# Performance work log

Hardware: AMD Instinct MI355X
Metric: run time of the kernel (lower is better)

The kernel has to match this reference:

```python
import jax, jax.numpy as jnp
import numpy as np

N_USER = 100000
N_ITEM = 100000
N_TAG = 10000
DIM = 128
E_BUYS = 1_000_000
E_REV = 1_000_000
E_TAGS = 1_000_000
W_SCALE = 0.05


def setup_inputs() -> dict:
    key = jax.random.key(0)
    ks = jax.random.split(key, 18)
    inp = {
        "x_user": jax.random.normal(ks[0], (N_USER, DIM), jnp.float32),
        "x_item": jax.random.normal(ks[1], (N_ITEM, DIM), jnp.float32),
        "x_tag": jax.random.normal(ks[2], (N_TAG, DIM), jnp.float32),
        # edge_index per relation: row 0 = src node ids, row 1 = dst node ids
        "ei_buys": jnp.stack([
            jax.random.randint(ks[3], (E_BUYS,), 0, N_USER, jnp.int32),
            jax.random.randint(ks[4], (E_BUYS,), 0, N_ITEM, jnp.int32)]),
        "ei_rev": jnp.stack([
            jax.random.randint(ks[5], (E_REV,), 0, N_ITEM, jnp.int32),
            jax.random.randint(ks[6], (E_REV,), 0, N_USER, jnp.int32)]),
        "ei_tags": jnp.stack([
            jax.random.randint(ks[7], (E_TAGS,), 0, N_TAG, jnp.int32),
            jax.random.randint(ks[8], (E_TAGS,), 0, N_ITEM, jnp.int32)]),
    }
    # SAGEConv params per edge type: lin_l (neighbor agg), lin_r (root), bias
    names = ["buys", "rev", "tags"]
    for i, n in enumerate(names):
        inp[f"Wl_{n}"] = jax.random.normal(ks[9 + 3 * i], (DIM, DIM), jnp.float32) * W_SCALE
        inp[f"Wr_{n}"] = jax.random.normal(ks[10 + 3 * i], (DIM, DIM), jnp.float32) * W_SCALE
        inp[f"b_{n}"] = jnp.zeros((DIM,), jnp.float32)
    return inp


def _sage(x_src, x_dst, ei, Wl, Wr, b):
    """SAGEConv with mean neighbor aggregation: lin_l(mean_j x_j) + lin_r(x_i) + b."""
    n_dst = x_dst.shape[0]
    src, dst = ei[0], ei[1]
    msg_sum = jax.ops.segment_sum(x_src[src], dst, num_segments=n_dst)  # [n_dst, D]
    cnt = jax.ops.segment_sum(jnp.ones(src.shape, x_src.dtype), dst, num_segments=n_dst)
    msg_mean = msg_sum / jnp.maximum(cnt, 1.0)[:, None]
    return msg_mean @ Wl + x_dst @ Wr + b


def reference(x_user, x_item, x_tag, ei_buys, ei_rev, ei_tags,
              Wl_buys, Wr_buys, b_buys,
              Wl_rev, Wr_rev, b_rev,
              Wl_tags, Wr_tags, b_tags):
    # per-relation SAGEConv
    o_item_buys = _sage(x_user, x_item, ei_buys, Wl_buys, Wr_buys, b_buys)
    o_user = _sage(x_item, x_user, ei_rev, Wl_rev, Wr_rev, b_rev)
    o_item_tags = _sage(x_tag, x_item, ei_tags, Wl_tags, Wr_tags, b_tags)
    # HeteroConv aggr='mean' across edge types per destination node type
    out_item = 0.5 * (o_item_buys + o_item_tags)
    out_user = o_user  # single relation into 'user'
    return (out_user, out_item)
```

## Files before the change

kernel.cpp:

```cpp
#include <hip/hip_runtime.h>
#include <hip/hip_bf16.h>
#include <stdint.h>

#define DIM 128
#define NNODE 100000
#define NB 196
#define NBT (3 * NB)
#define T_TILE 4096

typedef __attribute__((ext_vector_type(8))) short short8;
typedef __attribute__((ext_vector_type(4))) float f32x4;

__device__ __forceinline__ unsigned short f32_to_bf16_rne(float f) {
    union { float f; uint32_t u; } v; v.f = f;
    uint32_t u = v.u;
    uint32_t r = u + 0x7FFFu + ((u >> 16) & 1u);
    return (unsigned short)(r >> 16);
}
__device__ __forceinline__ float bf16_to_f32(unsigned short u) {
    union { uint32_t i; float f; } v; v.i = ((uint32_t)u) << 16; return v.f;
}

__global__ __launch_bounds__(256) void coarse_hist(
    const int* __restrict__ ei0, const int* __restrict__ ei1, const int* __restrict__ ei2,
    int E0, int E1, int E2, int* __restrict__ ccnt) {
    __shared__ int h[NBT];
    int Etot = E0 + E1 + E2;
    for (int i = threadIdx.x; i < NBT; i += 256) h[i] = 0;
    __syncthreads();
    for (int e = blockIdx.x * blockDim.x + threadIdx.x; e < Etot; e += gridDim.x * blockDim.x) {
        int rel, le; const int* ei; int E;
        if (e < E0)           { rel = 0; le = e;           ei = ei0; E = E0; }
        else if (e < E0 + E1) { rel = 1; le = e - E0;      ei = ei1; E = E1; }
        else                  { rel = 2; le = e - E0 - E1; ei = ei2; E = E2; }
        int d = ei[E + le];
        atomicAdd(&h[rel * NB + (d >> 9)], 1);
    }
    __syncthreads();
    for (int i = threadIdx.x; i < NBT; i += 256) {
        int c = h[i];
        if (c) atomicAdd(&ccnt[i], c);
    }
}

__global__ __launch_bounds__(1024) void coarse_scan(const int* __restrict__ ccnt,
                                                    int* __restrict__ bases,
                                                    int* __restrict__ cursor) {
    __shared__ int s[1024];
    int t = threadIdx.x;
    int v = (t < NBT) ? ccnt[t] : 0;
    s[t] = v;
    __syncthreads();
    for (int d = 1; d < 1024; d <<= 1) {
        int x = (t >= d) ? s[t - d] : 0;
        __syncthreads();
        s[t] += x;
        __syncthreads();
    }
    int excl = s[t] - v;
    if (t < NBT) { bases[t] = excl; cursor[t] = excl; }
    if (t == NBT) bases[NBT] = excl;
}

__global__ __launch_bounds__(256) void coarse_scatter(
    const int* __restrict__ ei0, const int* __restrict__ ei1, const int* __restrict__ ei2,
    int E0, int E1, int E2, int* __restrict__ cursor, int* __restrict__ pairs) {
    __shared__ int h[NBT], hb[NBT], lc[NBT];
    int Etot = E0 + E1 + E2;
    int ntiles = (Etot + T_TILE - 1) / T_TILE;
    for (int tile = blockIdx.x; tile < ntiles; tile += gridDim.x) {
        int tbase = tile * T_TILE;
        for (int i = threadIdx.x; i < NBT; i += 256) { h[i] = 0; lc[i] = 0; }
        __syncthreads();
        int binreg[16], valreg[16];
        #pragma unroll
        for (int k = 0; k < 16; k++) {
            int e = tbase + k * 256 + threadIdx.x;
            binreg[k] = -1;
            if (e < Etot) {
                int rel, le; const int* ei; int E;
                if (e < E0)           { rel = 0; le = e;           ei = ei0; E = E0; }
                else if (e < E0 + E1) { rel = 1; le = e - E0;      ei = ei1; E = E1; }
                else                  { rel = 2; le = e - E0 - E1; ei = ei2; E = E2; }
                int d = ei[E + le];
                int s = ei[le];
                int bin = rel * NB + (d >> 9);
                binreg[k] = bin;
                valreg[k] = s | ((d & 511) << 17);
                atomicAdd(&h[bin], 1);
            }
        }
        __syncthreads();
        for (int i = threadIdx.x; i < NBT; i += 256) {
            int c = h[i];
            hb[i] = c ? atomicAdd(&cursor[i], c) : 0;
        }
        __syncthreads();
        #pragma unroll
        for (int k = 0; k < 16; k++) {
            if (binreg[k] >= 0) {
                int bin = binreg[k];
                int pos = hb[bin] + atomicAdd(&lc[bin], 1);
                pairs[pos] = valreg[k];
            }
        }
        __syncthreads();
    }
}

__global__ __launch_bounds__(256) void fine_sort(
    const int* __restrict__ bases, const int* __restrict__ pairs,
    int* __restrict__ off, int* __restrict__ sorted, int N) {
    __shared__ int h[512], ho[512], ssum[256];
    int b = blockIdx.x;
    int rel = b / NB, jb = b - rel * NB;
    int ebase = bases[b], ne = bases[b + 1] - ebase;
    int dbase = jb << 9;
    int tid = threadIdx.x;
    for (int i = tid; i < 512; i += 256) h[i] = 0;
    __syncthreads();
    for (int i = tid; i < ne; i += 256) {
        int dl = pairs[ebase + i] >> 17;
        atomicAdd(&h[dl], 1);
    }
    __syncthreads();
    int v0 = h[tid * 2], v1 = h[tid * 2 + 1];
    int tsum = v0 + v1;
    ssum[tid] = tsum;
    __syncthreads();
    for (int s = 1; s < 256; s <<= 1) {
        int t = (tid >= s) ? ssum[tid - s] : 0;
        __syncthreads();
        ssum[tid] += t;
        __syncthreads();
    }
    int excl = ssum[tid] - tsum;
    ho[tid * 2] = excl;
    ho[tid * 2 + 1] = excl + v0;
    __syncthreads();
    for (int i = tid; i < 512; i += 256) {
        int d = dbase + i;
        if (d < N) off[rel * N + d] = ebase + ho[i];
        h[i] = 0;
    }
    __syncthreads();
    for (int i = tid; i < ne; i += 256) {
        int p = pairs[ebase + i];
        int dl = p >> 17;
        int pos = ebase + ho[dl] + atomicAdd(&h[dl], 1);
        sorted[pos] = p & 0x1FFFF;
    }
}

__global__ void pack_kernel(const float* __restrict__ Wl_b, const float* __restrict__ Wr_b,
                            const float* __restrict__ b_b,
                            const float* __restrict__ Wl_r, const float* __restrict__ Wr_r,
                            const float* __restrict__ b_r,
                            const float* __restrict__ Wl_t, const float* __restrict__ Wr_t,
                            const float* __restrict__ b_t,
                            unsigned short* __restrict__ pw_item,
                            unsigned short* __restrict__ pw_user,
                            float* __restrict__ bias_item, float* __restrict__ bias_user) {
    const int NI = 12 * 8 * 64 * 8;
    const int NU = 8 * 8 * 64 * 8;
    int o = blockIdx.x * blockDim.x + threadIdx.x;
    if (o < NI) {
        int j = o & 7, lane = (o >> 3) & 63, ks = o >> 12;
        int n = ((o >> 9) & 7) * 16 + (lane & 15);
        int k = (ks & 3) * 32 + (lane >> 4) * 8 + j;
        int src = ks >> 2;
        float v;
        if (src == 0)      v = 0.5f * Wl_b[k * DIM + n];
        else if (src == 1) v = 0.5f * Wl_t[k * DIM + n];
        else               v = 0.5f * (Wr_b[k * DIM + n] + Wr_t[k * DIM + n]);
        pw_item[o] = f32_to_bf16_rne(v);
    } else if (o < NI + NU) {
        int oo = o - NI;
        int j = oo & 7, lane = (oo >> 3) & 63, ks = oo >> 12;
        int n = ((oo >> 9) & 7) * 16 + (lane & 15);
        int k = (ks & 3) * 32 + (lane >> 4) * 8 + j;
        float v = ((ks >> 2) == 0) ? Wl_r[k * DIM + n] : Wr_r[k * DIM + n];
        pw_user[oo] = f32_to_bf16_rne(v);
    } else {
        int oo = o - NI - NU;
        if (oo < DIM)            bias_item[oo] = 0.5f * (b_b[oo] + b_t[oo]);
        else if (oo < 2 * DIM)   bias_user[oo - DIM] = b_r[oo - DIM];
    }
}

__device__ __forceinline__ void cg_product(
    unsigned char* stage, const short8* af,
    const unsigned short* __restrict__ pw, int slot0,
    const float* __restrict__ bias,
    unsigned short* __restrict__ dst, int g0, int lane) {
    const int quad = lane >> 4, l15 = lane & 15;
    f32x4 acc[8];
    #pragma unroll
    for (int i = 0; i < 8; i++) acc[i] = (f32x4){0.f, 0.f, 0.f, 0.f};
    #pragma unroll
    for (int ksl = 0; ksl < 4; ksl++) {
        const unsigned short* wp = pw + ((size_t)(slot0 + ksl) * 8 * 64 + lane) * 8;
        #pragma unroll
        for (int nt = 0; nt < 8; nt++) {
            short8 wfrag = *(const short8*)(wp + (size_t)nt * 64 * 8);
            acc[nt] = __builtin_amdgcn_mfma_f32_16x16x32_bf16(af[ksl], wfrag, acc[nt], 0, 0, 0);
        }
    }
    unsigned short* outb = (unsigned short*)stage;
    #pragma unroll
    for (int nt = 0; nt < 8; nt++) {
        float bv = bias ? bias[nt * 16 + l15] : 0.f;
        #pragma unroll
        for (int r = 0; r < 4; r++) {
            outb[(((quad << 2) + r) << 7) + (nt << 4) + l15] =
                f32_to_bf16_rne(acc[nt][r] + bv);
        }
    }
    unsigned char* mp = (unsigned char*)(dst + ((size_t)g0 << 7));
    #pragma unroll
    for (int s = 0; s < 4; s++) {
        uint4 vv = *(const uint4*)(stage + (s << 10) + (lane << 4));
        *(uint4*)(mp + (s << 10) + (lane << 4)) = vv;
    }
}

__global__ __launch_bounds__(256) void conv_gemm(
    const float* __restrict__ xu, const float* __restrict__ xi, const float* __restrict__ xt,
    const unsigned short* __restrict__ pw_item, const unsigned short* __restrict__ pw_user,
    const float* __restrict__ bias_item, const float* __restrict__ bias_user,
    unsigned short* __restrict__ yu, unsigned short* __restrict__ yi,
    unsigned short* __restrict__ yt,
    unsigned short* __restrict__ ru, unsigned short* __restrict__ ri,
    int GU, int GI, int GT) {
    __shared__ __align__(1024) unsigned char smem[4][4096];
    const int wid = threadIdx.x >> 6;
    const int lane = threadIdx.x & 63;
    const int grp = blockIdx.x * 4 + wid;
    if (grp >= GU + GI + GT) return;
    const float* src; const unsigned short *pwA, *pwB; const float* biasB;
    unsigned short *outA, *outB; int slotA, slotB, g0; bool two;
    if (grp < GU) {
        g0 = grp << 4; src = xu + ((size_t)g0 << 7);
        pwA = pw_item; slotA = 0; outA = yu;
        pwB = pw_user; slotB = 4; outB = ru; biasB = bias_user; two = true;
    } else if (grp < GU + GI) {
        g0 = (grp - GU) << 4; src = xi + ((size_t)g0 << 7);
        pwA = pw_user; slotA = 0; outA = yi;
        pwB = pw_item; slotB = 8; outB = ri; biasB = bias_item; two = true;
    } else {
        g0 = (grp - GU - GI) << 4; src = xt + ((size_t)g0 << 7);
        pwA = pw_item; slotA = 4; outA = yt; two = false;
        pwB = nullptr; outB = nullptr; biasB = nullptr; slotB = 0;
    }
    unsigned char* stage = smem[wid];
    #pragma unroll
    for (int s = 0; s < 8; s++) {
        float4 f = *(const float4*)((const unsigned char*)src + (s << 10) + (lane << 4));
        int row = (s << 1) + (lane >> 5);
        unsigned int b = ((unsigned int)row << 8) + ((unsigned int)(lane & 31) << 3);
        b ^= (unsigned int)((row & 15) << 4);
        ushort4 u;
        u.x = f32_to_bf16_rne(f.x); u.y = f32_to_bf16_rne(f.y);
        u.z = f32_to_bf16_rne(f.z); u.w = f32_to_bf16_rne(f.w);
        *(ushort4*)(stage + b) = u;
    }
    short8 af[4];
    const int quad = lane >> 4, l15 = lane & 15;
    #pragma unroll
    for (int ksl = 0; ksl < 4; ksl++) {
        unsigned int rb = ((unsigned int)l15 << 8) + (ksl << 6) + (quad << 4);
        rb ^= (unsigned int)(l15 << 4);
        af[ksl] = *(const short8*)(stage + rb);
    }
    cg_product(stage, af, pwA, slotA, nullptr, outA, g0, lane);
    if (two) cg_product(stage, af, pwB, slotB, biasB, outB, g0, lane);
}

__device__ __forceinline__ void gather_seg(
    const unsigned short* __restrict__ xs, const int* __restrict__ sorted,
    const int* bnd, unsigned char* stage, unsigned char* segb,
    int lane, int Etot, f32x4* acc) {
    const int b0 = bnd[0];
    const int L  = bnd[16] - b0;
    if (L <= 0) return;
    int nchunk = (L + 31) >> 5;
    if (nchunk > 20) nchunk = 20;
    const int tot = nchunk << 5;
    for (int i = lane; i < tot; i += 64) {
        int k = b0 + i;
        int s = 0;
        #pragma unroll
        for (int t = 1; t <= 16; t++) s += (k >= bnd[t]) ? 1 : 0;
        segb[i] = (unsigned char)s;
    }
    const int l15 = lane & 15;
    int deg = bnd[l15 + 1] - bnd[l15];
    const short ivb = (short)f32_to_bf16_rne(1.0f / (float)max(deg, 1));
    const int jsel = (lane & 7) >> 1;
    const int laneoff = ((lane >> 3) << 5) + ((lane & 1) << 4);
    const unsigned int stage_u =
        (unsigned int)(size_t)(__attribute__((address_space(3))) unsigned char*)stage;
    const unsigned int tbA = stage_u + ((lane >> 4) << 11) + ((lane & 15) << 3);
    const unsigned char* xsb = (const unsigned char*)xs;
    const int kmax = min(b0 + L - 1, Etot - 1);
    for (int c = 0; c < nchunk; c++) {
        int kk = min(b0 + (c << 5) + (lane & 31), kmax);
        const int sv = sorted[kk];
        #pragma unroll
        for (int q = 0; q < 8; q++) {
            int srow = __shfl(sv, (q << 2) + jsel, 64);
            const unsigned char* gp = xsb + (((size_t)srow) << 8) + laneoff;
            __builtin_amdgcn_global_load_lds(
                (const __attribute__((address_space(1))) unsigned int*)gp,
                (__attribute__((address_space(3))) unsigned int*)(stage + (q << 10)),
                16, 0, 0);
        }
        const unsigned long long sg =
            *(const unsigned long long*)(segb + (c << 5) + ((lane >> 4) << 3));
        short8 af;
        #pragma unroll
        for (int j = 0; j < 8; j++)
            af[j] = ((int)((sg >> (j << 3)) & 0xFFull) == l15) ? ivb : (short)0;
        asm volatile("s_waitcnt vmcnt(0)" ::: "memory");
        unsigned long long blo[8], bhi[8];
        #pragma unroll
        for (int nt = 0; nt < 8; nt++) {
            asm volatile("ds_read_b64_tr_b16 %0, %2\n\t"
                         "ds_read_b64_tr_b16 %1, %2 offset:1024"
                         : "=&v"(blo[nt]), "=&v"(bhi[nt]) : "v"(tbA + (nt << 7)));
        }
        asm volatile("s_waitcnt lgkmcnt(0)" ::: "memory");
        __builtin_amdgcn_sched_barrier(0);
        #pragma unroll
        for (int nt = 0; nt < 8; nt++) {
            union { unsigned long long u[2]; short8 s; } cv;
            cv.u[0] = blo[nt]; cv.u[1] = bhi[nt];
            acc[nt] = __builtin_amdgcn_mfma_f32_16x16x32_bf16(af, cv.s, acc[nt], 0, 0, 0);
        }
    }
}

__global__ __launch_bounds__(256) void agg_final(
    const unsigned short* __restrict__ yu, const unsigned short* __restrict__ yi,
    const unsigned short* __restrict__ yt,
    const unsigned short* __restrict__ ru, const unsigned short* __restrict__ ri,
    const int* __restrict__ sorted, const int* __restrict__ off,
    float* __restrict__ out, int N, int Etot) {
    __shared__ __align__(1024) unsigned char smem[4][9216];
    const int wid = threadIdx.x >> 6;
    const int lane = threadIdx.x & 63;
    const int grp = blockIdx.x * 4 + wid;
    const int Gi = N >> 4;
    if (grp >= 2 * Gi) return;
    unsigned char* stage = smem[wid];
    unsigned char* segb  = smem[wid] + 8192;
    int* bnd = (int*)(smem[wid] + 8192 + 640);
    const int quad = lane >> 4, l15 = lane & 15;

    f32x4 acc[8];
    #pragma unroll
    for (int i = 0; i < 8; i++) acc[i] = (f32x4){0.f, 0.f, 0.f, 0.f};

    float* op; const unsigned short* rt; int g0;
    if (grp < Gi) {
        g0 = grp << 4;
        if (lane < 17) bnd[lane] = off[g0 + lane];
        gather_seg(yu, sorted, bnd, stage, segb, lane, Etot, acc);
        if (lane < 17) { int idx = 2 * N + g0 + lane; bnd[lane] = (idx < 3 * N) ? off[idx] : Etot; }
        gather_seg(yt, sorted, bnd, stage, segb, lane, Etot, acc);
        op = out + (size_t)N * DIM; rt = ri;
    } else {
        g0 = (grp - Gi) << 4;
        if (lane < 17) bnd[lane] = off[N + g0 + lane];
        gather_seg(yi, sorted, bnd, stage, segb, lane, Etot, acc);
        op = out; rt = ru;
    }
    #pragma unroll
    for (int nt = 0; nt < 8; nt++) {
        #pragma unroll
        for (int r = 0; r < 4; r++) {
            size_t idx = (size_t)(g0 + (quad << 2) + r) * DIM + (nt << 4) + l15;
            op[idx] = acc[nt][r] + bf16_to_f32(rt[idx]);
        }
    }
}

extern "C" void kernel_launch(void* const* d_in, const int* in_sizes, int n_in,
                              void* d_out, int out_size, void* d_ws, size_t ws_size,
                              hipStream_t stream) {
    const float* x_user = (const float*)d_in[0];
    const float* x_item = (const float*)d_in[1];
    const float* x_tag  = (const float*)d_in[2];
    const int* ei_buys  = (const int*)d_in[3];
    const int* ei_rev   = (const int*)d_in[4];
    const int* ei_tags  = (const int*)d_in[5];
    const float* Wl_b = (const float*)d_in[6];
    const float* Wr_b = (const float*)d_in[7];
    const float* b_b  = (const float*)d_in[8];
    const float* Wl_r = (const float*)d_in[9];
    const float* Wr_r = (const float*)d_in[10];
    const float* b_r  = (const float*)d_in[11];
    const float* Wl_t = (const float*)d_in[12];
    const float* Wr_t = (const float*)d_in[13];
    const float* b_t  = (const float*)d_in[14];

    const int N  = NNODE;
    const int E0 = in_sizes[3] / 2, E1 = in_sizes[4] / 2, E2 = in_sizes[5] / 2;
    const int n_user = in_sizes[0] / DIM, n_item = in_sizes[1] / DIM, n_tag = in_sizes[2] / DIM;

    char* w = (char*)d_ws;
    int* off    = (int*)(w + 0);
    int* ccnt   = (int*)(w + 1200128);
    int* bases  = (int*)(w + 1202560);
    int* cursor = (int*)(w + 1204992);
    int* sorted = (int*)(w + 1207424);
    int* pairs  = (int*)(w + 13207424);
    unsigned short* pw_item = (unsigned short*)(w + 25207424);
    unsigned short* pw_user = (unsigned short*)(w + 25305728);
    float* bias_item = (float*)(w + 25371264);
    float* bias_user = (float*)(w + 25371776);
    unsigned short* yu = (unsigned short*)(w + 25372288);
    unsigned short* yi = (unsigned short*)(w + 50972288);
    unsigned short* yt = (unsigned short*)(w + 76572288);
    unsigned short* ru = (unsigned short*)(w + 79132288);
    unsigned short* ri = (unsigned short*)(w + 104732288);

    float* out_all = (float*)d_out;

    int Etot = E0 + E1 + E2;

    hipMemsetAsync(ccnt, 0, NBT * sizeof(int), stream);

    pack_kernel<<<(49152 + 32768 + 2 * DIM + 255) / 256, 256, 0, stream>>>(
        Wl_b, Wr_b, b_b, Wl_r, Wr_r, b_r, Wl_t, Wr_t, b_t,
        pw_item, pw_user, bias_item, bias_user);

    int GU = n_user / 16, GI = n_item / 16, GT = n_tag / 16;
    conv_gemm<<<(GU + GI + GT + 3) / 4, 256, 0, stream>>>(
        x_user, x_item, x_tag, pw_item, pw_user, bias_item, bias_user,
        yu, yi, yt, ru, ri, GU, GI, GT);

    coarse_hist<<<512, 256, 0, stream>>>(ei_buys, ei_rev, ei_tags, E0, E1, E2, ccnt);

    coarse_scan<<<1, 1024, 0, stream>>>(ccnt, bases, cursor);

    int ntiles = (Etot + T_TILE - 1) / T_TILE;
    coarse_scatter<<<ntiles, 256, 0, stream>>>(
        ei_buys, ei_rev, ei_tags, E0, E1, E2, cursor, pairs);

    fine_sort<<<NBT, 256, 0, stream>>>(bases, pairs, off, sorted, N);

    int ngrp = 2 * (N / 16);
    agg_final<<<(ngrp + 3) / 4, 256, 0, stream>>>(
        yu, yi, yt, ru, ri, sorted, off, out_all, N, Etot);
}
```

Measured before the change: 423.1 us.

## Fuse coarse histogram into conv GEMM launch and fold counter reset into pack

The coarse destination histogram is merged into the conv GEMM kernel as 512 extra leading blocks, so the two independent stages share one launch and can overlap on the GPU. The memset of the bucket counters moves into pack_kernel, removing a separate memset launch. The GEMM A-fragment load now reads fp32 rows straight from global memory into registers and converts them to bf16, skipping the LDS staging round-trip. The direct per-lane row loads are less coalesced than the old staged 1 KB strided loads, which could raise memory transaction cost for the 210k-row input read.

```diff
diff --git a/kernel.cpp b/kernel.cpp
--- a/kernel.cpp
+++ b/kernel.cpp
@@ -7,6 +7,7 @@
 #define NB 196
 #define NBT (3 * NB)
 #define T_TILE 4096
+#define NHIST 512
 
 typedef __attribute__((ext_vector_type(8))) short short8;
 typedef __attribute__((ext_vector_type(4))) float f32x4;
@@ -19,28 +20,6 @@
 }
 __device__ __forceinline__ float bf16_to_f32(unsigned short u) {
     union { uint32_t i; float f; } v; v.i = ((uint32_t)u) << 16; return v.f;
-}
-
-__global__ __launch_bounds__(256) void coarse_hist(
-    const int* __restrict__ ei0, const int* __restrict__ ei1, const int* __restrict__ ei2,
-    int E0, int E1, int E2, int* __restrict__ ccnt) {
-    __shared__ int h[NBT];
-    int Etot = E0 + E1 + E2;
-    for (int i = threadIdx.x; i < NBT; i += 256) h[i] = 0;
-    __syncthreads();
-    for (int e = blockIdx.x * blockDim.x + threadIdx.x; e < Etot; e += gridDim.x * blockDim.x) {
-        int rel, le; const int* ei; int E;
-        if (e < E0)           { rel = 0; le = e;           ei = ei0; E = E0; }
-        else if (e < E0 + E1) { rel = 1; le = e - E0;      ei = ei1; E = E1; }
-        else                  { rel = 2; le = e - E0 - E1; ei = ei2; E = E2; }
-        int d = ei[E + le];
-        atomicAdd(&h[rel * NB + (d >> 9)], 1);
-    }
-    __syncthreads();
-    for (int i = threadIdx.x; i < NBT; i += 256) {
-        int c = h[i];
-        if (c) atomicAdd(&ccnt[i], c);
-    }
 }
 
 __global__ __launch_bounds__(1024) void coarse_scan(const int* __restrict__ ccnt,
@@ -160,10 +139,12 @@
                             const float* __restrict__ b_t,
                             unsigned short* __restrict__ pw_item,
                             unsigned short* __restrict__ pw_user,
-                            float* __restrict__ bias_item, float* __restrict__ bias_user) {
+                            float* __restrict__ bias_item, float* __restrict__ bias_user,
+                            int* __restrict__ ccnt) {
     const int NI = 12 * 8 * 64 * 8;
     const int NU = 8 * 8 * 64 * 8;
     int o = blockIdx.x * blockDim.x + threadIdx.x;
+    if (o < NBT) ccnt[o] = 0;
     if (o < NI) {
         int j = o & 7, lane = (o >> 3) & 63, ks = o >> 12;
         int n = ((o >> 9) & 7) * 16 + (lane & 15);
@@ -224,18 +205,40 @@
     }
 }
 
-__global__ __launch_bounds__(256) void conv_gemm(
+__global__ __launch_bounds__(256) void prep_kernel(
     const float* __restrict__ xu, const float* __restrict__ xi, const float* __restrict__ xt,
     const unsigned short* __restrict__ pw_item, const unsigned short* __restrict__ pw_user,
     const float* __restrict__ bias_item, const float* __restrict__ bias_user,
     unsigned short* __restrict__ yu, unsigned short* __restrict__ yi,
     unsigned short* __restrict__ yt,
     unsigned short* __restrict__ ru, unsigned short* __restrict__ ri,
-    int GU, int GI, int GT) {
-    __shared__ __align__(1024) unsigned char smem[4][4096];
+    int GU, int GI, int GT,
+    const int* __restrict__ ei0, const int* __restrict__ ei1, const int* __restrict__ ei2,
+    int E0, int E1, int E2, int* __restrict__ ccnt) {
+    __shared__ __align__(1024) unsigned char smem[16384];
+    if (blockIdx.x < NHIST) {
+        int* h = (int*)smem;
+        int Etot = E0 + E1 + E2;
+        for (int i = threadIdx.x; i < NBT; i += 256) h[i] = 0;
+        __syncthreads();
+        for (int e = blockIdx.x * 256 + threadIdx.x; e < Etot; e += NHIST * 256) {
+            int rel, le; const int* ei; int E;
+            if (e < E0)           { rel = 0; le = e;           ei = ei0; E = E0; }
+            else if (e < E0 + E1) { rel = 1; le = e - E0;      ei = ei1; E = E1; }
+            else                  { rel = 2; le = e - E0 - E1; ei = ei2; E = E2; }
+            int d = ei[E + le];
+            atomicAdd(&h[rel * NB + (d >> 9)], 1);
+        }
+        __syncthreads();
+        for (int i = threadIdx.x; i < NBT; i += 256) {
+            int c = h[i];
+            if (c) atomicAdd(&ccnt[i], c);
+        }
+        return;
+    }
     const int wid = threadIdx.x >> 6;
     const int lane = threadIdx.x & 63;
-    const int grp = blockIdx.x * 4 + wid;
+    const int grp = (blockIdx.x - NHIST) * 4 + wid;
     if (grp >= GU + GI + GT) return;
     const float* src; const unsigned short *pwA, *pwB; const float* biasB;
     unsigned short *outA, *outB; int slotA, slotB, g0; bool two;
@@ -252,25 +255,21 @@
         pwA = pw_item; slotA = 4; outA = yt; two = false;
         pwB = nullptr; outB = nullptr; biasB = nullptr; slotB = 0;
     }
-    unsigned char* stage = smem[wid];
-    #pragma unroll
-    for (int s = 0; s < 8; s++) {
-        float4 f = *(const float4*)((const unsigned char*)src + (s << 10) + (lane << 4));
-        int row = (s << 1) + (lane >> 5);
-        unsigned int b = ((unsigned int)row << 8) + ((unsigned int)(lane & 31) << 3);
-        b ^= (unsigned int)((row & 15) << 4);
-        ushort4 u;
-        u.x = f32_to_bf16_rne(f.x); u.y = f32_to_bf16_rne(f.y);
-        u.z = f32_to_bf16_rne(f.z); u.w = f32_to_bf16_rne(f.w);
-        *(ushort4*)(stage + b) = u;
-    }
+    unsigned char* stage = smem + wid * 4096;
+    const int quad = lane >> 4, l15 = lane & 15;
+    const float* rowp = src + (size_t)l15 * DIM;
     short8 af[4];
-    const int quad = lane >> 4, l15 = lane & 15;
     #pragma unroll
     for (int ksl = 0; ksl < 4; ksl++) {
-        unsigned int rb = ((unsigned int)l15 << 8) + (ksl << 6) + (quad << 4);
-        rb ^= (unsigned int)(l15 << 4);
-        af[ksl] = *(const short8*)(stage + rb);
+        const float* p = rowp + ksl * 32 + quad * 8;
+        float4 a = *(const float4*)p;
+        float4 b = *(const float4*)(p + 4);
+        short8 f;
+        f[0] = (short)f32_to_bf16_rne(a.x); f[1] = (short)f32_to_bf16_rne(a.y);
+        f[2] = (short)f32_to_bf16_rne(a.z); f[3] = (short)f32_to_bf16_rne(a.w);
+        f[4] = (short)f32_to_bf16_rne(b.x); f[5] = (short)f32_to_bf16_rne(b.y);
+        f[6] = (short)f32_to_bf16_rne(b.z); f[7] = (short)f32_to_bf16_rne(b.w);
+        af[ksl] = f;
     }
     cg_product(stage, af, pwA, slotA, nullptr, outA, g0, lane);
     if (two) cg_product(stage, af, pwB, slotB, biasB, outB, g0, lane);
@@ -429,18 +428,16 @@
 
     int Etot = E0 + E1 + E2;
 
-    hipMemsetAsync(ccnt, 0, NBT * sizeof(int), stream);
-
     pack_kernel<<<(49152 + 32768 + 2 * DIM + 255) / 256, 256, 0, stream>>>(
         Wl_b, Wr_b, b_b, Wl_r, Wr_r, b_r, Wl_t, Wr_t, b_t,
-        pw_item, pw_user, bias_item, bias_user);
+        pw_item, pw_user, bias_item, bias_user, ccnt);
 
     int GU = n_user / 16, GI = n_item / 16, GT = n_tag / 16;
-    conv_gemm<<<(GU + GI + GT + 3) / 4, 256, 0, stream>>>(
+    int conv_blocks = (GU + GI + GT + 3) / 4;
+    prep_kernel<<<NHIST + conv_blocks, 256, 0, stream>>>(
         x_user, x_item, x_tag, pw_item, pw_user, bias_item, bias_user,
-        yu, yi, yt, ru, ri, GU, GI, GT);
-
-    coarse_hist<<<512, 256, 0, stream>>>(ei_buys, ei_rev, ei_tags, E0, E1, E2, ccnt);
+        yu, yi, yt, ru, ri, GU, GI, GT,
+        ei_buys, ei_rev, ei_tags, E0, E1, E2, ccnt);
 
     coarse_scan<<<1, 1024, 0, stream>>>(ccnt, bases, cursor);
 
```

Result: no change. 416.2 us (-1.6%).
